# Optimization experiments

Hardware: AMD Instinct MI355X
Metric: run time of the kernel (lower is better)

Reference implementation:

```python
import jax, jax.numpy as jnp
import numpy as np

USER_NUM = 100000
ITEM_NUM = 50000
EMB_SIZE = 64
N_LAYERS = 3
N_EDGES = 2400000
N_NODES = USER_NUM + ITEM_NUM


def setup_inputs() -> dict:
    key = jax.random.key(0)
    k1, k2, k3, k4, k5 = jax.random.split(key, 5)
    user_emb = jax.random.normal(k1, (USER_NUM, EMB_SIZE), dtype=jnp.float32)
    item_emb = jax.random.normal(k2, (ITEM_NUM, EMB_SIZE), dtype=jnp.float32)
    adj_rows = jax.random.randint(k3, (N_EDGES,), 0, N_NODES, dtype=jnp.int32)
    adj_cols = jax.random.randint(k4, (N_EDGES,), 0, N_NODES, dtype=jnp.int32)
    # normalized adjacency values (positive, ~1/sqrt(deg_i*deg_j) scale)
    adj_vals = jax.random.uniform(k5, (N_EDGES,), dtype=jnp.float32) * 0.1
    return {"user_emb": user_emb, "item_emb": item_emb,
            "adj_rows": adj_rows, "adj_cols": adj_cols, "adj_vals": adj_vals}


def reference(user_emb, item_emb, adj_rows, adj_cols, adj_vals):
    # ego: [N_NODES, emb]
    ego = jnp.concatenate([user_emb, item_emb], axis=0)
    acc = jnp.zeros_like(ego)
    for _ in range(N_LAYERS):
        # SpMM: out[r] += vals[e] * ego[cols[e]] over all edges e with rows[e]==r
        msgs = adj_vals[:, None] * ego[adj_cols]          # [E, emb]
        ego = jax.ops.segment_sum(msgs, adj_rows, num_segments=N_NODES)
        acc = acc + ego
    mean_emb = acc / N_LAYERS                              # mean over stacked layers
    return mean_emb[:USER_NUM], mean_emb[USER_NUM:]
```

## Files before the change

### kernel.cpp

```cpp
#include <hip/hip_runtime.h>

#define USER_NUM 100000
#define ITEM_NUM 50000
#define N_NODES (USER_NUM + ITEM_NUM)
#define EMB 64
#define N_EDGES 2400000
#define N_LAYERS 3

#define RPB 512
#define RL_SH 9
#define NB 293
#define ROW_PAD 150016

#define NCHUNK_A 256
#define CH_A 9375

#define CH2 4096
#define NCHUNK2 ((N_EDGES + CH2 - 1) / CH2)
#define CONCAT_BLOCKS 1024

#define VAL_ENC 163840.0f
#define VAL_DEC (1.0f / 163840.0f)

typedef unsigned short u16;
typedef unsigned int u32;

__device__ __forceinline__ float bf2f(u16 h) {
    return __uint_as_float(((unsigned)h) << 16);
}
__device__ __forceinline__ u16 f2bf(float f) {
    unsigned u = __float_as_uint(f);
    unsigned r = 0x7FFFu + ((u >> 16) & 1u);
    return (u16)((u + r) >> 16);
}

__global__ __launch_bounds__(256) void count_kernel(const int* __restrict__ rows,
                                                    int* __restrict__ cnt) {
    __shared__ int hist[NB];
    const int t = threadIdx.x;
    const int k = blockIdx.x;
    for (int b = t; b < NB; b += 256) hist[b] = 0;
    __syncthreads();
    const int cbase = k * CH_A;
    const int cend = min(cbase + CH_A, N_EDGES);
    for (int i = cbase + t; i < cend; i += 256) {
        atomicAdd(&hist[rows[i] >> RL_SH], 1);
    }
    __syncthreads();
    for (int b = t; b < NB; b += 256) cnt[k * NB + b] = hist[b];
}

__global__ __launch_bounds__(256) void bucket_scan(const int* __restrict__ cnt,
                                                   int* __restrict__ bstart,
                                                   int* __restrict__ gcursor) {
    __shared__ int tot[NB];
    __shared__ int sums[256];
    const int t = threadIdx.x;
    for (int b = t; b < NB; b += 256) {
        int v = 0;
        for (int k = 0; k < NCHUNK_A; ++k) v += cnt[k * NB + b];
        tot[b] = v;
    }
    __syncthreads();
    const int own0 = t * 2;
    int h0 = (own0 < NB) ? tot[own0] : 0;
    int h1 = (own0 + 1 < NB) ? tot[own0 + 1] : 0;
    sums[t] = h0 + h1;
    __syncthreads();
    for (int off = 1; off < 256; off <<= 1) {
        int x = 0;
        if (t >= off) x = sums[t - off];
        __syncthreads();
        sums[t] += x;
        __syncthreads();
    }
    int run = (t == 0) ? 0 : sums[t - 1];
    if (own0 < NB) { bstart[own0] = run; gcursor[own0] = run; }
    if (own0 + 1 < NB) { bstart[own0 + 1] = run + h0; gcursor[own0 + 1] = run + h0; }
    if (t == 255) bstart[NB] = N_EDGES;
}

__global__ __launch_bounds__(512) void scatter_and_concat(
        const int* __restrict__ rows, const int* __restrict__ cols,
        const float* __restrict__ vals, int* __restrict__ gcursor,
        u32* __restrict__ ecr, u16* __restrict__ ev,
        const float* __restrict__ user_emb, const float* __restrict__ item_emb,
        u16* __restrict__ ego) {
    const int t = threadIdx.x;
    if (blockIdx.x >= NCHUNK2) {
        const int n4 = (N_NODES * EMB) / 4;
        const int user4 = (USER_NUM * EMB) / 4;
        const int blk = blockIdx.x - NCHUNK2;
        for (int i = blk * 512 + t; i < n4; i += CONCAT_BLOCKS * 512) {
            float4 v;
            if (i < user4) {
                v = reinterpret_cast<const float4*>(user_emb)[i];
            } else {
                v = reinterpret_cast<const float4*>(item_emb)[i - user4];
            }
            ushort4 o;
            o.x = f2bf(v.x); o.y = f2bf(v.y); o.z = f2bf(v.z); o.w = f2bf(v.w);
            reinterpret_cast<ushort4*>(ego)[i] = o;
        }
        return;
    }

    __shared__ int hist[NB];
    __shared__ int base[NB];
    __shared__ u32 se_cr[CH2];
    __shared__ u32 se_vb[CH2];
    __shared__ int sums[512];

    const int cbase = blockIdx.x * CH2;
    const int cend = min(cbase + CH2, N_EDGES) - cbase;

    if (t < NB) hist[t] = 0;
    __syncthreads();
    for (int i = t; i < cend; i += 512) {
        atomicAdd(&hist[rows[cbase + i] >> RL_SH], 1);
    }
    __syncthreads();

    const int h0 = (t < NB) ? hist[t] : 0;
    sums[t] = h0;
    __syncthreads();
    for (int off = 1; off < 512; off <<= 1) {
        int x = 0;
        if (t >= off) x = sums[t - off];
        __syncthreads();
        sums[t] += x;
        __syncthreads();
    }
    if (t < NB) base[t] = sums[t] - h0;
    __syncthreads();

    if (t < NB) {
        int g = 0;
        if (h0) g = atomicAdd(&gcursor[t], h0);
        hist[t] = g - base[t];
    }
    __syncthreads();

    for (int i = t; i < cend; i += 512) {
        const int r = rows[cbase + i];
        const int c = cols[cbase + i];
        const float v = vals[cbase + i];
        const int b = r >> RL_SH;
        int q = __float2int_rn(v * VAL_ENC);
        q = min(q, 16383);
        const int slot = atomicAdd(&base[b], 1);
        se_cr[slot] = (u32)c | ((u32)(r & (RPB - 1)) << 18);
        se_vb[slot] = ((u32)q << 16) | (u32)b;
    }
    __syncthreads();

    for (int i = t; i < cend; i += 512) {
        const u32 vb = se_vb[i];
        const int gb = hist[vb & 0xFFFF];
        ecr[gb + i] = se_cr[i];
        ev[gb + i] = (u16)(vb >> 16);
    }
}

__global__ __launch_bounds__(512) void row_sort(const u32* __restrict__ ecr,
                                                const u16* __restrict__ ev,
                                                const int* __restrict__ bstart,
                                                int* __restrict__ offsets,
                                                u32* __restrict__ edges_out) {
    __shared__ int cnt[RPB];
    __shared__ int cur[RPB];
    const int t = threadIdx.x;
    const int b = blockIdx.x;
    const int s0 = bstart[b];
    const int s1 = bstart[b + 1];

    cnt[t] = 0;
    __syncthreads();
    for (int e = s0 + t; e < s1; e += 512)
        atomicAdd(&cnt[ecr[e] >> 18], 1);
    __syncthreads();

    const int c0 = cnt[t];
    cur[t] = c0;
    __syncthreads();
    for (int off = 1; off < 512; off <<= 1) {
        int x = 0;
        if (t >= off) x = cur[t - off];
        __syncthreads();
        cur[t] += x;
        __syncthreads();
    }
    const int ex = cur[t] - c0;
    cur[t] = ex;
    offsets[b * RPB + t] = s0 + ex;
    __syncthreads();

    for (int e = s0 + t; e < s1; e += 512) {
        const u32 cr = ecr[e];
        const int rl = cr >> 18;
        const int pos = s0 + atomicAdd(&cur[rl], 1);
        edges_out[pos] = (cr & 0x3FFFF) | ((u32)ev[e] << 18);
    }
    if (b == NB - 1 && t == 0) offsets[ROW_PAD] = N_EDGES;
}

__device__ __forceinline__ float4 row_sum8(const u32* __restrict__ edges,
                                           const u16* __restrict__ x,
                                           int start, int end, int d0) {
    float4 s = {0.f, 0.f, 0.f, 0.f};
    for (int e0 = start; e0 < end; e0 += 8) {
        u32 E[8];
#pragma unroll
        for (int j = 0; j < 8; ++j) {
            const int ee = e0 + j;
            E[j] = edges[ee < end ? ee : end - 1];
        }
        ushort4 X[8];
#pragma unroll
        for (int j = 0; j < 8; ++j) {
            X[j] = *reinterpret_cast<const ushort4*>(
                x + (size_t)(E[j] & 0x3FFFF) * EMB + d0);
        }
#pragma unroll
        for (int j = 0; j < 8; ++j) {
            const float v = (e0 + j < end) ? (float)(E[j] >> 18) * VAL_DEC : 0.f;
            s.x += v * bf2f(X[j].x);
            s.y += v * bf2f(X[j].y);
            s.z += v * bf2f(X[j].z);
            s.w += v * bf2f(X[j].w);
        }
    }
    return s;
}

__global__ __launch_bounds__(256) void spmm_gather_bf16(
        const int* __restrict__ offsets, const u32* __restrict__ edges,
        const u16* __restrict__ x, u16* __restrict__ y) {
    const int wid = threadIdx.x >> 6;
    const int lane = threadIdx.x & 63;
    const int sub = lane >> 4;
    const int l16 = lane & 15;
    const int r = blockIdx.x * 16 + wid * 4 + sub;
    if (r >= N_NODES) return;

    const int start = offsets[r];
    const int end = offsets[r + 1];
    const int d0 = 4 * l16;
    const float4 s = row_sum8(edges, x, start, end, d0);

    ushort4 o;
    o.x = f2bf(s.x); o.y = f2bf(s.y); o.z = f2bf(s.z); o.w = f2bf(s.w);
    *reinterpret_cast<ushort4*>(y + (size_t)r * EMB + d0) = o;
}

__global__ __launch_bounds__(256) void spmm_final(
        const int* __restrict__ offsets, const u32* __restrict__ edges,
        const u16* __restrict__ x, const u16* __restrict__ y1,
        const u16* __restrict__ y2, float* __restrict__ out) {
    const int wid = threadIdx.x >> 6;
    const int lane = threadIdx.x & 63;
    const int sub = lane >> 4;
    const int l16 = lane & 15;
    const int r = blockIdx.x * 16 + wid * 4 + sub;
    if (r >= N_NODES) return;

    const int start = offsets[r];
    const int end = offsets[r + 1];
    const int d0 = 4 * l16;
    const float4 s = row_sum8(edges, x, start, end, d0);

    const size_t o = (size_t)r * EMB + d0;
    const ushort4 a = *reinterpret_cast<const ushort4*>(y1 + o);
    const ushort4 b = *reinterpret_cast<const ushort4*>(y2 + o);
    const float sc = 1.0f / N_LAYERS;
    float4 ov;
    ov.x = (bf2f(a.x) + bf2f(b.x) + s.x) * sc;
    ov.y = (bf2f(a.y) + bf2f(b.y) + s.y) * sc;
    ov.z = (bf2f(a.z) + bf2f(b.z) + s.z) * sc;
    ov.w = (bf2f(a.w) + bf2f(b.w) + s.w) * sc;
    *reinterpret_cast<float4*>(out + o) = ov;
}

extern "C" void kernel_launch(void* const* d_in, const int* in_sizes, int n_in,
                              void* d_out, int out_size, void* d_ws, size_t ws_size,
                              hipStream_t stream) {
    const float* user_emb = (const float*)d_in[0];
    const float* item_emb = (const float*)d_in[1];
    const int*   adj_rows = (const int*)d_in[2];
    const int*   adj_cols = (const int*)d_in[3];
    const float* adj_vals = (const float*)d_in[4];
    float* out = (float*)d_out;

    const size_t nodeElems = (size_t)N_NODES * EMB;

    u16* b0 = (u16*)d_ws;
    u16* b1 = b0 + nodeElems;
    u16* b2 = b1 + nodeElems;
    u32* ecr = (u32*)(b2 + nodeElems);
    u16* ev = (u16*)(ecr + N_EDGES);
    u32* edges_final = (u32*)(ev + N_EDGES);
    int* unionReg = (int*)(edges_final + N_EDGES);
    int* cnt = unionReg;
    int* offsets = unionReg;
    int* bstart = unionReg + 150024;
    int* gcursor = bstart + (NB + 1);

    count_kernel<<<NCHUNK_A, 256, 0, stream>>>(adj_rows, cnt);
    bucket_scan<<<1, 256, 0, stream>>>(cnt, bstart, gcursor);
    scatter_and_concat<<<NCHUNK2 + CONCAT_BLOCKS, 512, 0, stream>>>(
        adj_rows, adj_cols, adj_vals, gcursor, ecr, ev,
        user_emb, item_emb, b0);
    row_sort<<<NB, 512, 0, stream>>>(ecr, ev, bstart, offsets, edges_final);

    const int spmmGrid = (N_NODES + 15) / 16;
    spmm_gather_bf16<<<spmmGrid, 256, 0, stream>>>(offsets, edges_final, b0, b1);
    spmm_gather_bf16<<<spmmGrid, 256, 0, stream>>>(offsets, edges_final, b1, b2);
    spmm_final<<<spmmGrid, 256, 0, stream>>>(offsets, edges_final, b2, b1, b2, out);
}
```

Measured before the change: 225.0 us.

## Scatter edges directly to global buckets and widen row_sort blocks to 1024 threads

Removes the block-local prefix scan and shared-memory staging in the scatter kernel; each edge now claims its global position with a shared atomic on the per-bucket cursor and writes straight to global memory. This saves shared memory and several barriers, but the global writes are less coalesced than the staged, bucket-contiguous writes were. Separately, row_sort runs with 1024 threads per block so each of the 293 buckets is processed by more threads.

```diff
diff --git a/kernel.cpp b/kernel.cpp
--- a/kernel.cpp
+++ b/kernel.cpp
@@ -106,10 +106,6 @@
     }
 
     __shared__ int hist[NB];
-    __shared__ int base[NB];
-    __shared__ u32 se_cr[CH2];
-    __shared__ u32 se_vb[CH2];
-    __shared__ int sums[512];
 
     const int cbase = blockIdx.x * CH2;
     const int cend = min(cbase + CH2, N_EDGES) - cbase;
@@ -121,23 +117,11 @@
     }
     __syncthreads();
 
-    const int h0 = (t < NB) ? hist[t] : 0;
-    sums[t] = h0;
-    __syncthreads();
-    for (int off = 1; off < 512; off <<= 1) {
-        int x = 0;
-        if (t >= off) x = sums[t - off];
-        __syncthreads();
-        sums[t] += x;
-        __syncthreads();
-    }
-    if (t < NB) base[t] = sums[t] - h0;
-    __syncthreads();
-
     if (t < NB) {
+        const int h0 = hist[t];
         int g = 0;
         if (h0) g = atomicAdd(&gcursor[t], h0);
-        hist[t] = g - base[t];
+        hist[t] = g;
     }
     __syncthreads();
 
@@ -148,25 +132,17 @@
         const int b = r >> RL_SH;
         int q = __float2int_rn(v * VAL_ENC);
         q = min(q, 16383);
-        const int slot = atomicAdd(&base[b], 1);
-        se_cr[slot] = (u32)c | ((u32)(r & (RPB - 1)) << 18);
-        se_vb[slot] = ((u32)q << 16) | (u32)b;
-    }
-    __syncthreads();
-
-    for (int i = t; i < cend; i += 512) {
-        const u32 vb = se_vb[i];
-        const int gb = hist[vb & 0xFFFF];
-        ecr[gb + i] = se_cr[i];
-        ev[gb + i] = (u16)(vb >> 16);
-    }
-}
-
-__global__ __launch_bounds__(512) void row_sort(const u32* __restrict__ ecr,
-                                                const u16* __restrict__ ev,
-                                                const int* __restrict__ bstart,
-                                                int* __restrict__ offsets,
-                                                u32* __restrict__ edges_out) {
+        const int pos = atomicAdd(&hist[b], 1);
+        ecr[pos] = (u32)c | ((u32)(r & (RPB - 1)) << 18);
+        ev[pos] = (u16)q;
+    }
+}
+
+__global__ __launch_bounds__(1024) void row_sort(const u32* __restrict__ ecr,
+                                                 const u16* __restrict__ ev,
+                                                 const int* __restrict__ bstart,
+                                                 int* __restrict__ offsets,
+                                                 u32* __restrict__ edges_out) {
     __shared__ int cnt[RPB];
     __shared__ int cur[RPB];
     const int t = threadIdx.x;
@@ -174,28 +150,30 @@
     const int s0 = bstart[b];
     const int s1 = bstart[b + 1];
 
-    cnt[t] = 0;
-    __syncthreads();
-    for (int e = s0 + t; e < s1; e += 512)
+    if (t < RPB) cnt[t] = 0;
+    __syncthreads();
+    for (int e = s0 + t; e < s1; e += 1024)
         atomicAdd(&cnt[ecr[e] >> 18], 1);
     __syncthreads();
 
-    const int c0 = cnt[t];
-    cur[t] = c0;
-    __syncthreads();
-    for (int off = 1; off < 512; off <<= 1) {
+    const int c0 = (t < RPB) ? cnt[t] : 0;
+    if (t < RPB) cur[t] = c0;
+    __syncthreads();
+    for (int off = 1; off < RPB; off <<= 1) {
         int x = 0;
-        if (t >= off) x = cur[t - off];
-        __syncthreads();
-        cur[t] += x;
-        __syncthreads();
-    }
-    const int ex = cur[t] - c0;
-    cur[t] = ex;
-    offsets[b * RPB + t] = s0 + ex;
-    __syncthreads();
-
-    for (int e = s0 + t; e < s1; e += 512) {
+        if (t < RPB && t >= off) x = cur[t - off];
+        __syncthreads();
+        if (t < RPB) cur[t] += x;
+        __syncthreads();
+    }
+    if (t < RPB) {
+        const int ex = cur[t] - c0;
+        cur[t] = ex;
+        offsets[b * RPB + t] = s0 + ex;
+    }
+    __syncthreads();
+
+    for (int e = s0 + t; e < s1; e += 1024) {
         const u32 cr = ecr[e];
         const int rl = cr >> 18;
         const int pos = s0 + atomicAdd(&cur[rl], 1);
@@ -310,7 +288,7 @@
     scatter_and_concat<<<NCHUNK2 + CONCAT_BLOCKS, 512, 0, stream>>>(
         adj_rows, adj_cols, adj_vals, gcursor, ecr, ev,
         user_emb, item_emb, b0);
-    row_sort<<<NB, 512, 0, stream>>>(ecr, ev, bstart, offsets, edges_final);
+    row_sort<<<NB, 1024, 0, stream>>>(ecr, ev, bstart, offsets, edges_final);
 
     const int spmmGrid = (N_NODES + 15) / 16;
     spmm_gather_bf16<<<spmmGrid, 256, 0, stream>>>(offsets, edges_final, b0, b1);
```

Measured after the change: 243.3 us. +8.1%, slower.
